# Optimization experiments

Hardware: AMD Instinct MI355X
Metric: run time of the kernel (lower is better)

## Reference

```python
import jax, jax.numpy as jnp
import numpy as np

DIM = 512
HEADS = 8
DIM_HEAD = 64
INNER = HEADS * DIM_HEAD
SCALE = DIM_HEAD ** -0.5


def setup_inputs() -> dict:
    key = jax.random.key(0)
    ks = jax.random.split(key, 7)
    B, N = 8, 1024
    x = jax.random.normal(ks[0], (B, N, DIM), dtype=jnp.float32)
    rel_pos_bias = jax.random.normal(ks[1], (HEADS, N, N), dtype=jnp.float32) * 0.02
    w_qkv = jax.random.normal(ks[2], (DIM, 3 * INNER), dtype=jnp.float32) * (DIM ** -0.5)
    w_out = jax.random.normal(ks[3], (INNER, DIM), dtype=jnp.float32) * (INNER ** -0.5)
    b_out = jnp.zeros((DIM,), dtype=jnp.float32)
    ln_gamma = jnp.ones((DIM,), dtype=jnp.float32)
    ln_beta = jnp.zeros((DIM,), dtype=jnp.float32)
    return {"x": x, "rel_pos_bias": rel_pos_bias, "w_qkv": w_qkv,
            "w_out": w_out, "b_out": b_out, "ln_gamma": ln_gamma, "ln_beta": ln_beta}


def _layernorm(x, gamma, beta, eps=1e-5):
    mu = jnp.mean(x, axis=-1, keepdims=True)
    var = jnp.var(x, axis=-1, keepdims=True)
    return (x - mu) * jax.lax.rsqrt(var + eps) * gamma + beta


def reference(x, rel_pos_bias, w_qkv, w_out, b_out, ln_gamma, ln_beta):
    B, N, _ = x.shape
    xn = _layernorm(x, ln_gamma, ln_beta)
    qkv = xn @ w_qkv  # [B,N,3*INNER]
    q, k, v = jnp.split(qkv, 3, axis=-1)
    # b n (h d) -> b h n d
    reshape = lambda t: t.reshape(B, N, HEADS, DIM_HEAD).transpose(0, 2, 1, 3)
    q, k, v = reshape(q) * SCALE, reshape(k), reshape(v)
    sim = jnp.einsum('bhid,bhjd->bhij', q, k)
    sim = sim + rel_pos_bias  # broadcast [h,N,N] over batch
    attn = jax.nn.softmax(sim, axis=-1)
    out = jnp.einsum('bhij,bhjd->bhid', attn, v)
    out = out.transpose(0, 2, 1, 3).reshape(B, N, INNER)
    return out @ w_out + b_out
```

## Files before the change

kernel.cpp:

```cpp
#include <hip/hip_runtime.h>
#include <hip/hip_bf16.h>

#define DIM 512
#define HEADS 8
#define DHEAD 64
#define INNER 512
#define NSEQ 1024
#define BATCH 8
#define MROWS (BATCH*NSEQ)
#define QK_SCALE 0.125f

typedef __attribute__((ext_vector_type(4))) float f32x4;
typedef __attribute__((ext_vector_type(8))) short short8;
typedef unsigned short ushort_t;

__device__ inline ushort_t f2bf(float f) {
    __hip_bfloat16 h = __float2bfloat16(f);
    return *reinterpret_cast<ushort_t*>(&h);
}
__device__ inline float bf2f(ushort_t u) {
    union { unsigned int i; float f; } c; c.i = ((unsigned int)u) << 16; return c.f;
}

__global__ __launch_bounds__(256) void ln_kernel(const float* __restrict__ x,
        const float* __restrict__ gamma, const float* __restrict__ beta,
        ushort_t* __restrict__ xn) {
    int row = blockIdx.x * 4 + (threadIdx.x >> 6);
    int lane = threadIdx.x & 63;
    const float4* xr = (const float4*)(x + (size_t)row * DIM);
    float4 a0 = xr[lane];
    float4 a1 = xr[lane + 64];
    float s  = a0.x + a0.y + a0.z + a0.w + a1.x + a1.y + a1.z + a1.w;
    float ss = a0.x*a0.x + a0.y*a0.y + a0.z*a0.z + a0.w*a0.w
             + a1.x*a1.x + a1.y*a1.y + a1.z*a1.z + a1.w*a1.w;
    for (int off = 1; off < 64; off <<= 1) {
        s  += __shfl_xor(s, off);
        ss += __shfl_xor(ss, off);
    }
    float mean = s * (1.0f / DIM);
    float var  = ss * (1.0f / DIM) - mean * mean;
    float inv  = rsqrtf(var + 1e-5f);
    const float4* g4 = (const float4*)gamma;
    const float4* b4 = (const float4*)beta;
    float4 g0 = g4[lane], g1 = g4[lane + 64];
    float4 be0 = b4[lane], be1 = b4[lane + 64];
    ushort4 o0, o1;
    o0.x = f2bf((a0.x - mean) * inv * g0.x + be0.x);
    o0.y = f2bf((a0.y - mean) * inv * g0.y + be0.y);
    o0.z = f2bf((a0.z - mean) * inv * g0.z + be0.z);
    o0.w = f2bf((a0.w - mean) * inv * g0.w + be0.w);
    o1.x = f2bf((a1.x - mean) * inv * g1.x + be1.x);
    o1.y = f2bf((a1.y - mean) * inv * g1.y + be1.y);
    o1.z = f2bf((a1.z - mean) * inv * g1.z + be1.z);
    o1.w = f2bf((a1.w - mean) * inv * g1.w + be1.w);
    ushort4* outr = (ushort4*)(xn + (size_t)row * DIM);
    outr[lane] = o0;
    outr[lane + 64] = o1;
}

__global__ __launch_bounds__(256) void transpose_cast(const float* __restrict__ w,
        ushort_t* __restrict__ wt, int ncols) {
    int idx = blockIdx.x * 256 + threadIdx.x;
    int n = idx >> 9, k = idx & 511;
    wt[idx] = f2bf(w[(size_t)k * ncols + n]);
}

__global__ __launch_bounds__(256) void bias_cvt(const float* __restrict__ in,
        ushort_t* __restrict__ out) {
    int i = blockIdx.x * 256 + threadIdx.x;
    float4 v = ((const float4*)in)[i];
    ushort4 o;
    o.x = f2bf(v.x); o.y = f2bf(v.y); o.z = f2bf(v.z); o.w = f2bf(v.w);
    ((ushort4*)out)[i] = o;
}

__global__ __launch_bounds__(256) void v_transpose(const ushort_t* __restrict__ vb,
        ushort_t* __restrict__ vt) {
    __shared__ ushort_t T[64][72];
    int bh = blockIdx.y;
    int s0 = blockIdx.x * 64;
    int t = threadIdx.x;
    int row = t >> 2, c = (t & 3) * 16;
    const ushort_t* src = vb + ((size_t)bh * NSEQ + s0 + row) * DHEAD + c;
    *(uint4*)&T[row][c]     = *(const uint4*)(src);
    *(uint4*)&T[row][c + 8] = *(const uint4*)(src + 8);
    __syncthreads();
    int d = t >> 2;
    int sq = (t & 3) * 16;
    ushort_t tmp[16];
    for (int j = 0; j < 16; j++) tmp[j] = T[sq + j][d];
    *(uint4*)(vt + ((size_t)bh * DHEAD + d) * NSEQ + s0 + sq)     = *(uint4*)&tmp[0];
    *(uint4*)(vt + ((size_t)bh * DHEAD + d) * NSEQ + s0 + sq + 8) = *(uint4*)&tmp[8];
}

template<int EPI>
__global__ __launch_bounds__(256) void gemm_kernel(
        const ushort_t* __restrict__ A, const ushort_t* __restrict__ Bt,
        ushort_t* __restrict__ qb, ushort_t* __restrict__ kb, ushort_t* __restrict__ vb,
        float* __restrict__ outp, const float* __restrict__ bvec) {
    __shared__ ushort_t Als[128][40];
    __shared__ ushort_t Bls[128][40];
    int t = threadIdx.x;
    int bm = blockIdx.y, bn = blockIdx.x;
    int lane = t & 63, w = t >> 6, wm = w >> 1, wn = w & 1;
    int l15 = lane & 15, l4 = lane >> 4;
    f32x4 acc[4][4] = {};

    for (int kt = 0; kt < DIM / 32; ++kt) {
        __syncthreads();
        {
            int row = t >> 2, c8 = (t & 3) * 8;
            uint4 va0 = *(const uint4*)(A  + (size_t)(bm*128 + row)      * DIM + kt*32 + c8);
            uint4 va1 = *(const uint4*)(A  + (size_t)(bm*128 + row + 64) * DIM + kt*32 + c8);
            uint4 vb0 = *(const uint4*)(Bt + (size_t)(bn*128 + row)      * DIM + kt*32 + c8);
            uint4 vb1 = *(const uint4*)(Bt + (size_t)(bn*128 + row + 64) * DIM + kt*32 + c8);
            *(uint4*)&Als[row][c8]      = va0;
            *(uint4*)&Als[row + 64][c8] = va1;
            *(uint4*)&Bls[row][c8]      = vb0;
            *(uint4*)&Bls[row + 64][c8] = vb1;
        }
        __syncthreads();
        short8 af[4], bfr[4];
        for (int mi = 0; mi < 4; mi++) af[mi]  = *(const short8*)&Als[wm*64 + mi*16 + l15][l4*8];
        for (int ni = 0; ni < 4; ni++) bfr[ni] = *(const short8*)&Bls[wn*64 + ni*16 + l15][l4*8];
        for (int mi = 0; mi < 4; mi++)
            for (int ni = 0; ni < 4; ni++)
                acc[mi][ni] = __builtin_amdgcn_mfma_f32_16x16x32_bf16(af[mi], bfr[ni], acc[mi][ni], 0, 0, 0);
    }

    int rbase = bm*128 + wm*64 + l4*4;
    int cbase = bn*128 + wn*64 + l15;
    for (int mi = 0; mi < 4; mi++)
        for (int ni = 0; ni < 4; ni++) {
            int c = cbase + ni*16;
            for (int j = 0; j < 4; j++) {
                int r = rbase + mi*16 + j;
                float val = acc[mi][ni][j];
                if (EPI == 0) {
                    int part = c >> 9, cw = c & 511;
                    int h = cw >> 6, d = cw & 63;
                    int b = r >> 10, i = r & 1023;
                    size_t off = (((size_t)(b*HEADS + h)) * NSEQ + i) * DHEAD + d;
                    if (part == 0)      qb[off] = f2bf(val * QK_SCALE);
                    else if (part == 1) kb[off] = f2bf(val);
                    else                vb[off] = f2bf(val);
                } else {
                    outp[(size_t)r * DIM + c] = val + bvec[c];
                }
            }
        }
}

__global__ __launch_bounds__(256) void attn_kernel(
        const ushort_t* __restrict__ q, const ushort_t* __restrict__ k,
        const ushort_t* __restrict__ vt, const ushort_t* __restrict__ biasb,
        ushort_t* __restrict__ attno) {
    __shared__ ushort_t Kls[64][72];
    __shared__ ushort_t Vtls[64][72];
    __shared__ ushort_t Pls[4][16][72];
    int t = threadIdx.x, lane = t & 63, w = t >> 6;
    int l15 = lane & 15, l4 = lane >> 4;
    int b = blockIdx.z, h = blockIdx.y, q0 = blockIdx.x * 64;
    size_t bh = (size_t)(b * HEADS + h);
    const ushort_t* qp = q  + (bh * NSEQ + q0 + w*16) * DHEAD;
    const ushort_t* kp = k  + bh * NSEQ * DHEAD;
    const ushort_t* vp = vt + bh * DHEAD * NSEQ;
    int qrow = q0 + w*16 + l15;
    const ushort_t* bp = biasb + ((size_t)h * NSEQ + qrow) * NSEQ;

    short8 bq[2];
    bq[0] = *(const short8*)(qp + l15*DHEAD + l4*8);
    bq[1] = *(const short8*)(qp + l15*DHEAD + l4*8 + 32);

    f32x4 o[4] = {};
    float mrun = -INFINITY, lrun = 0.f;

    int srow = t >> 2, sc = (t & 3) * 16;

    for (int kt = 0; kt < NSEQ / 64; ++kt) {
        __syncthreads();
        {
            const ushort_t* ks = kp + (size_t)(kt*64 + srow) * DHEAD + sc;
            const ushort_t* vs = vp + (size_t)srow * NSEQ + kt*64 + sc;
            *(uint4*)&Kls[srow][sc]      = *(const uint4*)(ks);
            *(uint4*)&Kls[srow][sc + 8]  = *(const uint4*)(ks + 8);
            *(uint4*)&Vtls[srow][sc]     = *(const uint4*)(vs);
            *(uint4*)&Vtls[srow][sc + 8] = *(const uint4*)(vs + 8);
        }
        __syncthreads();

        f32x4 s[4];
        for (int ni = 0; ni < 4; ni++) {
            f32x4 z = {};
            short8 ak0 = *(const short8*)&Kls[ni*16 + l15][l4*8];
            short8 ak1 = *(const short8*)&Kls[ni*16 + l15][l4*8 + 32];
            z = __builtin_amdgcn_mfma_f32_16x16x32_bf16(ak0, bq[0], z, 0, 0, 0);
            z = __builtin_amdgcn_mfma_f32_16x16x32_bf16(ak1, bq[1], z, 0, 0, 0);
            s[ni] = z;
        }

        float p[16];
        float mj = -INFINITY;
        for (int ni = 0; ni < 4; ni++) {
            ushort4 b4 = *(const ushort4*)(bp + kt*64 + ni*16 + l4*4);
            float v0 = s[ni][0] + bf2f(b4.x);
            float v1 = s[ni][1] + bf2f(b4.y);
            float v2 = s[ni][2] + bf2f(b4.z);
            float v3 = s[ni][3] + bf2f(b4.w);
            p[ni*4+0] = v0; p[ni*4+1] = v1; p[ni*4+2] = v2; p[ni*4+3] = v3;
            mj = fmaxf(mj, fmaxf(fmaxf(v0, v1), fmaxf(v2, v3)));
        }
        mj = fmaxf(mj, __shfl_xor(mj, 16));
        mj = fmaxf(mj, __shfl_xor(mj, 32));
        float mnew = fmaxf(mrun, mj);
        float scl = __expf(mrun - mnew);
        float rs = 0.f;
        for (int i = 0; i < 16; i++) {
            p[i] = __expf(p[i] - mnew);
            rs += p[i];
        }
        rs += __shfl_xor(rs, 16);
        rs += __shfl_xor(rs, 32);
        lrun = lrun * scl + rs;
        mrun = mnew;
        for (int di = 0; di < 4; di++) o[di] *= scl;

        for (int ni = 0; ni < 4; ni++) {
            ushort4 pk;
            pk.x = f2bf(p[ni*4+0]); pk.y = f2bf(p[ni*4+1]);
            pk.z = f2bf(p[ni*4+2]); pk.w = f2bf(p[ni*4+3]);
            *(ushort4*)&Pls[w][l15][ni*16 + l4*4] = pk;
        }

        for (int ks2 = 0; ks2 < 2; ks2++) {
            short8 pb = *(const short8*)&Pls[w][l15][ks2*32 + l4*8];
            for (int di = 0; di < 4; di++) {
                short8 av = *(const short8*)&Vtls[di*16 + l15][ks2*32 + l4*8];
                o[di] = __builtin_amdgcn_mfma_f32_16x16x32_bf16(av, pb, o[di], 0, 0, 0);
            }
        }
    }

    float inv = 1.0f / lrun;
    for (int di = 0; di < 4; di++) {
        ushort4 ov;
        ov.x = f2bf(o[di][0] * inv);
        ov.y = f2bf(o[di][1] * inv);
        ov.z = f2bf(o[di][2] * inv);
        ov.w = f2bf(o[di][3] * inv);
        *(ushort4*)(attno + ((size_t)(b*NSEQ + qrow)) * INNER + h*DHEAD + di*16 + l4*4) = ov;
    }
}

extern "C" void kernel_launch(void* const* d_in, const int* in_sizes, int n_in,
                              void* d_out, int out_size, void* d_ws, size_t ws_size,
                              hipStream_t stream) {
    (void)in_sizes; (void)n_in; (void)out_size; (void)ws_size;
    const float* x      = (const float*)d_in[0];
    const float* bias   = (const float*)d_in[1];
    const float* w_qkv  = (const float*)d_in[2];
    const float* w_out  = (const float*)d_in[3];
    const float* b_out  = (const float*)d_in[4];
    const float* gamma  = (const float*)d_in[5];
    const float* beta   = (const float*)d_in[6];
    float* out = (float*)d_out;

    ushort_t* xn    = (ushort_t*)d_ws;
    ushort_t* wqkvT = xn + (size_t)MROWS * DIM;
    ushort_t* woutT = wqkvT + (size_t)1536 * 512;
    ushort_t* qb    = woutT + (size_t)512 * 512;
    ushort_t* kb    = qb + (size_t)MROWS * INNER;
    ushort_t* vb    = kb + (size_t)MROWS * INNER;
    ushort_t* vt    = vb + (size_t)MROWS * INNER;
    ushort_t* attn  = vt + (size_t)MROWS * INNER;
    ushort_t* biasb = attn + (size_t)MROWS * INNER;

    hipLaunchKernelGGL(ln_kernel, dim3(MROWS / 4), dim3(256), 0, stream, x, gamma, beta, xn);
    hipLaunchKernelGGL(transpose_cast, dim3(1536 * 512 / 256), dim3(256), 0, stream, w_qkv, wqkvT, 3 * INNER);
    hipLaunchKernelGGL(transpose_cast, dim3(512 * 512 / 256), dim3(256), 0, stream, w_out, woutT, DIM);
    hipLaunchKernelGGL(bias_cvt, dim3(HEADS * NSEQ * NSEQ / 4 / 256), dim3(256), 0, stream, bias, biasb);
    hipLaunchKernelGGL((gemm_kernel<0>), dim3(1536 / 128, MROWS / 128), dim3(256), 0, stream,
                       xn, wqkvT, qb, kb, vb, nullptr, nullptr);
    hipLaunchKernelGGL(v_transpose, dim3(NSEQ / 64, BATCH * HEADS), dim3(256), 0, stream, vb, vt);
    hipLaunchKernelGGL(attn_kernel, dim3(NSEQ / 64, HEADS, BATCH), dim3(256), 0, stream,
                       qb, kb, vt, biasb, attn);
    hipLaunchKernelGGL((gemm_kernel<1>), dim3(DIM / 128, MROWS / 128), dim3(256), 0, stream,
                       attn, woutT, nullptr, nullptr, nullptr, out, b_out);
}
```

Before: 211.3 us.

## Tile weight transpose, widen GEMM K-tile, prefetch K/V, lazy softmax rescale

The weight transpose-cast now goes through a shared-memory tile, so both the fp32 reads and the bf16 writes are coalesced instead of strided. The GEMM uses a 64-wide K step with swapped MFMA operands, which lets the epilogue write vectorized ushort4/float4 stores; it also raises wave priority around the MFMA loops. The attention kernel prefetches the next K/V tile into registers while computing the current one. It also skips the online-softmax rescale unless the new row max exceeds the running max by more than 8, trading some exp headroom for fewer multiplies on the output accumulators.

```diff
diff --git a/kernel.cpp b/kernel.cpp
--- a/kernel.cpp
+++ b/kernel.cpp
@@ -60,9 +60,28 @@
 
 __global__ __launch_bounds__(256) void transpose_cast(const float* __restrict__ w,
         ushort_t* __restrict__ wt, int ncols) {
-    int idx = blockIdx.x * 256 + threadIdx.x;
-    int n = idx >> 9, k = idx & 511;
-    wt[idx] = f2bf(w[(size_t)k * ncols + n]);
+    __shared__ ushort_t T[64][72];
+    int n0 = blockIdx.x * 64, k0 = blockIdx.y * 64;
+    int t = threadIdx.x;
+    int kr = t >> 2;
+    int nc = (t & 3) * 16;
+    const float4* src = (const float4*)(w + (size_t)(k0 + kr) * ncols + n0 + nc);
+    float4 f0 = src[0], f1 = src[1], f2 = src[2], f3 = src[3];
+    ushort_t tmp[16];
+    tmp[0]=f2bf(f0.x); tmp[1]=f2bf(f0.y); tmp[2]=f2bf(f0.z); tmp[3]=f2bf(f0.w);
+    tmp[4]=f2bf(f1.x); tmp[5]=f2bf(f1.y); tmp[6]=f2bf(f1.z); tmp[7]=f2bf(f1.w);
+    tmp[8]=f2bf(f2.x); tmp[9]=f2bf(f2.y); tmp[10]=f2bf(f2.z); tmp[11]=f2bf(f2.w);
+    tmp[12]=f2bf(f3.x); tmp[13]=f2bf(f3.y); tmp[14]=f2bf(f3.z); tmp[15]=f2bf(f3.w);
+    *(uint4*)&T[kr][nc]     = *(uint4*)&tmp[0];
+    *(uint4*)&T[kr][nc + 8] = *(uint4*)&tmp[8];
+    __syncthreads();
+    int nr = t >> 2;
+    int kc = (t & 3) * 16;
+    ushort_t o[16];
+    for (int j = 0; j < 16; j++) o[j] = T[kc + j][nr];
+    ushort_t* dst = wt + (size_t)(n0 + nr) * 512 + k0 + kc;
+    *(uint4*)(dst)     = *(uint4*)&o[0];
+    *(uint4*)(dst + 8) = *(uint4*)&o[8];
 }
 
 __global__ __launch_bounds__(256) void bias_cvt(const float* __restrict__ in,
@@ -98,57 +117,82 @@
         const ushort_t* __restrict__ A, const ushort_t* __restrict__ Bt,
         ushort_t* __restrict__ qb, ushort_t* __restrict__ kb, ushort_t* __restrict__ vb,
         float* __restrict__ outp, const float* __restrict__ bvec) {
-    __shared__ ushort_t Als[128][40];
-    __shared__ ushort_t Bls[128][40];
+    __shared__ ushort_t Als[128][72];
+    __shared__ ushort_t Bls[128][72];
     int t = threadIdx.x;
     int bm = blockIdx.y, bn = blockIdx.x;
     int lane = t & 63, w = t >> 6, wm = w >> 1, wn = w & 1;
     int l15 = lane & 15, l4 = lane >> 4;
     f32x4 acc[4][4] = {};
-
-    for (int kt = 0; kt < DIM / 32; ++kt) {
+    int srow = t >> 1;
+    int sc   = (t & 1) * 32;
+
+    for (int kt = 0; kt < DIM / 64; ++kt) {
         __syncthreads();
         {
-            int row = t >> 2, c8 = (t & 3) * 8;
-            uint4 va0 = *(const uint4*)(A  + (size_t)(bm*128 + row)      * DIM + kt*32 + c8);
-            uint4 va1 = *(const uint4*)(A  + (size_t)(bm*128 + row + 64) * DIM + kt*32 + c8);
-            uint4 vb0 = *(const uint4*)(Bt + (size_t)(bn*128 + row)      * DIM + kt*32 + c8);
-            uint4 vb1 = *(const uint4*)(Bt + (size_t)(bn*128 + row + 64) * DIM + kt*32 + c8);
-            *(uint4*)&Als[row][c8]      = va0;
-            *(uint4*)&Als[row + 64][c8] = va1;
-            *(uint4*)&Bls[row][c8]      = vb0;
-            *(uint4*)&Bls[row + 64][c8] = vb1;
+            const ushort_t* ap = A  + (size_t)(bm*128 + srow) * DIM + kt*64 + sc;
+            const ushort_t* bp = Bt + (size_t)(bn*128 + srow) * DIM + kt*64 + sc;
+            uint4 a0 = *(const uint4*)(ap);
+            uint4 a1 = *(const uint4*)(ap + 8);
+            uint4 a2 = *(const uint4*)(ap + 16);
+            uint4 a3 = *(const uint4*)(ap + 24);
+            uint4 b0 = *(const uint4*)(bp);
+            uint4 b1 = *(const uint4*)(bp + 8);
+            uint4 b2 = *(const uint4*)(bp + 16);
+            uint4 b3 = *(const uint4*)(bp + 24);
+            *(uint4*)&Als[srow][sc]      = a0;
+            *(uint4*)&Als[srow][sc + 8]  = a1;
+            *(uint4*)&Als[srow][sc + 16] = a2;
+            *(uint4*)&Als[srow][sc + 24] = a3;
+            *(uint4*)&Bls[srow][sc]      = b0;
+            *(uint4*)&Bls[srow][sc + 8]  = b1;
+            *(uint4*)&Bls[srow][sc + 16] = b2;
+            *(uint4*)&Bls[srow][sc + 24] = b3;
         }
         __syncthreads();
-        short8 af[4], bfr[4];
-        for (int mi = 0; mi < 4; mi++) af[mi]  = *(const short8*)&Als[wm*64 + mi*16 + l15][l4*8];
-        for (int ni = 0; ni < 4; ni++) bfr[ni] = *(const short8*)&Bls[wn*64 + ni*16 + l15][l4*8];
-        for (int mi = 0; mi < 4; mi++)
-            for (int ni = 0; ni < 4; ni++)
-                acc[mi][ni] = __builtin_amdgcn_mfma_f32_16x16x32_bf16(af[mi], bfr[ni], acc[mi][ni], 0, 0, 0);
-    }
-
-    int rbase = bm*128 + wm*64 + l4*4;
-    int cbase = bn*128 + wn*64 + l15;
-    for (int mi = 0; mi < 4; mi++)
+        for (int ks = 0; ks < 2; ks++) {
+            short8 af[4], bfr[4];
+            for (int mi = 0; mi < 4; mi++) af[mi]  = *(const short8*)&Als[wm*64 + mi*16 + l15][ks*32 + l4*8];
+            for (int ni = 0; ni < 4; ni++) bfr[ni] = *(const short8*)&Bls[wn*64 + ni*16 + l15][ks*32 + l4*8];
+            __builtin_amdgcn_s_setprio(1);
+            for (int mi = 0; mi < 4; mi++)
+                for (int ni = 0; ni < 4; ni++)
+                    acc[mi][ni] = __builtin_amdgcn_mfma_f32_16x16x32_bf16(bfr[ni], af[mi], acc[mi][ni], 0, 0, 0);
+            __builtin_amdgcn_s_setprio(0);
+        }
+    }
+
+    for (int mi = 0; mi < 4; mi++) {
+        int r = bm*128 + wm*64 + mi*16 + l15;
         for (int ni = 0; ni < 4; ni++) {
-            int c = cbase + ni*16;
-            for (int j = 0; j < 4; j++) {
-                int r = rbase + mi*16 + j;
-                float val = acc[mi][ni][j];
-                if (EPI == 0) {
-                    int part = c >> 9, cw = c & 511;
-                    int h = cw >> 6, d = cw & 63;
-                    int b = r >> 10, i = r & 1023;
-                    size_t off = (((size_t)(b*HEADS + h)) * NSEQ + i) * DHEAD + d;
-                    if (part == 0)      qb[off] = f2bf(val * QK_SCALE);
-                    else if (part == 1) kb[off] = f2bf(val);
-                    else                vb[off] = f2bf(val);
+            int c = bn*128 + wn*64 + ni*16 + l4*4;
+            f32x4 v = acc[mi][ni];
+            if (EPI == 0) {
+                int part = c >> 9, cw = c & 511;
+                int h = cw >> 6, d = cw & 63;
+                int b = r >> 10, i = r & 1023;
+                size_t off = (((size_t)(b*HEADS + h)) * NSEQ + i) * DHEAD + d;
+                ushort4 o;
+                if (part == 0) {
+                    o.x = f2bf(v[0] * QK_SCALE); o.y = f2bf(v[1] * QK_SCALE);
+                    o.z = f2bf(v[2] * QK_SCALE); o.w = f2bf(v[3] * QK_SCALE);
+                    *(ushort4*)(qb + off) = o;
+                } else if (part == 1) {
+                    o.x = f2bf(v[0]); o.y = f2bf(v[1]); o.z = f2bf(v[2]); o.w = f2bf(v[3]);
+                    *(ushort4*)(kb + off) = o;
                 } else {
-                    outp[(size_t)r * DIM + c] = val + bvec[c];
+                    o.x = f2bf(v[0]); o.y = f2bf(v[1]); o.z = f2bf(v[2]); o.w = f2bf(v[3]);
+                    *(ushort4*)(vb + off) = o;
                 }
+            } else {
+                float4 bv = *(const float4*)(bvec + c);
+                float4 o2;
+                o2.x = v[0] + bv.x; o2.y = v[1] + bv.y;
+                o2.z = v[2] + bv.z; o2.w = v[3] + bv.w;
+                *(float4*)(outp + (size_t)r * DIM + c) = o2;
             }
         }
+    }
 }
 
 __global__ __launch_bounds__(256) void attn_kernel(
@@ -177,19 +221,35 @@
 
     int srow = t >> 2, sc = (t & 3) * 16;
 
+    uint4 kreg0, kreg1, vreg0, vreg1;
+    {
+        const ushort_t* ks0 = kp + (size_t)srow * DHEAD + sc;
+        const ushort_t* vs0 = vp + (size_t)srow * NSEQ + sc;
+        kreg0 = *(const uint4*)(ks0);
+        kreg1 = *(const uint4*)(ks0 + 8);
+        vreg0 = *(const uint4*)(vs0);
+        vreg1 = *(const uint4*)(vs0 + 8);
+    }
+
     for (int kt = 0; kt < NSEQ / 64; ++kt) {
         __syncthreads();
-        {
-            const ushort_t* ks = kp + (size_t)(kt*64 + srow) * DHEAD + sc;
-            const ushort_t* vs = vp + (size_t)srow * NSEQ + kt*64 + sc;
-            *(uint4*)&Kls[srow][sc]      = *(const uint4*)(ks);
-            *(uint4*)&Kls[srow][sc + 8]  = *(const uint4*)(ks + 8);
-            *(uint4*)&Vtls[srow][sc]     = *(const uint4*)(vs);
-            *(uint4*)&Vtls[srow][sc + 8] = *(const uint4*)(vs + 8);
-        }
+        *(uint4*)&Kls[srow][sc]      = kreg0;
+        *(uint4*)&Kls[srow][sc + 8]  = kreg1;
+        *(uint4*)&Vtls[srow][sc]     = vreg0;
+        *(uint4*)&Vtls[srow][sc + 8] = vreg1;
         __syncthreads();
 
+        if (kt + 1 < NSEQ / 64) {
+            const ushort_t* ksn = kp + (size_t)((kt+1)*64 + srow) * DHEAD + sc;
+            const ushort_t* vsn = vp + (size_t)srow * NSEQ + (kt+1)*64 + sc;
+            kreg0 = *(const uint4*)(ksn);
+            kreg1 = *(const uint4*)(ksn + 8);
+            vreg0 = *(const uint4*)(vsn);
+            vreg1 = *(const uint4*)(vsn + 8);
+        }
+
         f32x4 s[4];
+        __builtin_amdgcn_s_setprio(1);
         for (int ni = 0; ni < 4; ni++) {
             f32x4 z = {};
             short8 ak0 = *(const short8*)&Kls[ni*16 + l15][l4*8];
@@ -198,6 +258,7 @@
             z = __builtin_amdgcn_mfma_f32_16x16x32_bf16(ak1, bq[1], z, 0, 0, 0);
             s[ni] = z;
         }
+        __builtin_amdgcn_s_setprio(0);
 
         float p[16];
         float mj = -INFINITY;
@@ -212,18 +273,21 @@
         }
         mj = fmaxf(mj, __shfl_xor(mj, 16));
         mj = fmaxf(mj, __shfl_xor(mj, 32));
-        float mnew = fmaxf(mrun, mj);
-        float scl = __expf(mrun - mnew);
+        if (!__all(mj <= mrun + 8.f)) {
+            float mnew = fmaxf(mrun, mj);
+            float scl = __expf(mrun - mnew);
+            lrun *= scl;
+            for (int di = 0; di < 4; di++) o[di] *= scl;
+            mrun = mnew;
+        }
         float rs = 0.f;
         for (int i = 0; i < 16; i++) {
-            p[i] = __expf(p[i] - mnew);
+            p[i] = __expf(p[i] - mrun);
             rs += p[i];
         }
         rs += __shfl_xor(rs, 16);
         rs += __shfl_xor(rs, 32);
-        lrun = lrun * scl + rs;
-        mrun = mnew;
-        for (int di = 0; di < 4; di++) o[di] *= scl;
+        lrun += rs;
 
         for (int ni = 0; ni < 4; ni++) {
             ushort4 pk;
@@ -232,6 +296,7 @@
             *(ushort4*)&Pls[w][l15][ni*16 + l4*4] = pk;
         }
 
+        __builtin_amdgcn_s_setprio(1);
         for (int ks2 = 0; ks2 < 2; ks2++) {
             short8 pb = *(const short8*)&Pls[w][l15][ks2*32 + l4*8];
             for (int di = 0; di < 4; di++) {
@@ -239,6 +304,7 @@
                 o[di] = __builtin_amdgcn_mfma_f32_16x16x32_bf16(av, pb, o[di], 0, 0, 0);
             }
         }
+        __builtin_amdgcn_s_setprio(0);
     }
 
     float inv = 1.0f / lrun;
@@ -276,8 +342,8 @@
     ushort_t* biasb = attn + (size_t)MROWS * INNER;
 
     hipLaunchKernelGGL(ln_kernel, dim3(MROWS / 4), dim3(256), 0, stream, x, gamma, beta, xn);
-    hipLaunchKernelGGL(transpose_cast, dim3(1536 * 512 / 256), dim3(256), 0, stream, w_qkv, wqkvT, 3 * INNER);
-    hipLaunchKernelGGL(transpose_cast, dim3(512 * 512 / 256), dim3(256), 0, stream, w_out, woutT, DIM);
+    hipLaunchKernelGGL(transpose_cast, dim3(1536 / 64, 512 / 64), dim3(256), 0, stream, w_qkv, wqkvT, 3 * INNER);
+    hipLaunchKernelGGL(transpose_cast, dim3(512 / 64, 512 / 64), dim3(256), 0, stream, w_out, woutT, DIM);
     hipLaunchKernelGGL(bias_cvt, dim3(HEADS * NSEQ * NSEQ / 4 / 256), dim3(256), 0, stream, bias, biasb);
     hipLaunchKernelGGL((gemm_kernel<0>), dim3(1536 / 128, MROWS / 128), dim3(256), 0, stream,
                        xn, wqkvT, qb, kb, vb, nullptr, nullptr);
```

Result: faster. 203.8 us (-3.6%).
